# Optimization experiments

Measured on AMD Instinct MI355X. Metric: run time of the kernel, lower is better.

## Reference

```python
import jax, jax.numpy as jnp
import numpy as np

HEADS, DIM_HEAD, BITS = 12, 64, 4


def quantize(q, bits):
    # per-tensor affine fake-quant, exactly as the torch quantize()
    s = (q.max() - q.min()) / (2.0 ** bits - 1.0)
    z = jnp.round(2.0 ** bits - 1.0 - q.max() / s)
    return jnp.round(q / s + z), s, z


def setup_inputs() -> dict:
    key = jax.random.key(0)
    k1, k2, k3, k4 = jax.random.split(key, 4)
    return {
        "x": jax.random.normal(k1, (4, 1024, 768), jnp.float32),
        "w_qkv": jax.random.normal(k2, (2304, 768), jnp.float32) * 0.02,  # torch Linear weight [out,in]
        "w_out": jax.random.normal(k3, (768, 768), jnp.float32) * 0.02,
        "b_out": jax.random.normal(k4, (768,), jnp.float32) * 0.02,
    }


def reference(x, w_qkv, w_out, b_out):
    scale = DIM_HEAD ** -0.5
    B, N, D = x.shape
    # --- quantized QKV projection: x @ W^T with zero-point correction ---
    xq, sx1, zx1 = quantize(x, BITS)
    w1, sw1, zw1 = quantize(w_qkv.T, BITS)  # [D, 3*inner]
    xqkv = (xq @ w1
            - w1.sum(0, keepdims=True) * zx1
            - xq.sum(2, keepdims=True) * zw1
            + zx1 * zw1 * D) * (sx1 * sw1)  # [B, N, 3*inner]
    q, k, v = jnp.split(xqkv, 3, axis=-1)
    to_heads = lambda t: t.reshape(B, N, HEADS, DIM_HEAD).transpose(0, 2, 1, 3)  # b h n d
    q, k, v = to_heads(q), to_heads(k), to_heads(v)
    # --- quantized QK^T (note: original omits the +zq*zk*d term) ---
    qq, sq, zq = quantize(q, BITS)
    kq, sk, zk = quantize(k.transpose(0, 1, 3, 2), BITS)  # b h d n
    dots = (qq @ kq
            - kq.sum(2, keepdims=True) * zq
            - qq.sum(3, keepdims=True) * zk) * (scale * sq * sk)  # b h n n
    a = jax.nn.softmax(dots, axis=-1)
    # --- quantized A @ V ---
    aq, sa, za = quantize(a, BITS)
    vq, sv, zv = quantize(v, BITS)
    out = (aq @ vq
           - vq.sum(2, keepdims=True) * za
           - aq.sum(3, keepdims=True) * zv
           + za * zv * N) * (sa * sv)  # b h n d
    out = out.transpose(0, 2, 1, 3).reshape(B, N, HEADS * DIM_HEAD)
    # --- quantized output projection (faithful to original: correction uses
    # xqkv.sum / xqkv width, reproducing the source's use of `x` here) ---
    oq, sx2, zx2 = quantize(out, BITS)
    w2, sw2, zw2 = quantize(w_out.T, BITS)  # [inner, D]
    o = (oq @ w2
         - w2.sum(0, keepdims=True) * zx2
         - xqkv.sum(2, keepdims=True) * zw2
         + zx2 * zw2 * xqkv.shape[2]) * (sx2 * sw2) + b_out
    return o
```

## Files before the change

kernel.cpp:

```cpp
#include <hip/hip_runtime.h>
#include <math.h>

#define HEADS 12
#define DH    64
#define Dm    768
#define I3    2304
#define Nn    1024
#define Mm    4096
#define BHt   48

#define P_X  0
#define P_W1 1
#define P_Q  2
#define P_K  3
#define P_V  4
#define P_A  5
#define P_O  6
#define P_W2 7

typedef int v4i __attribute__((ext_vector_type(4)));

__device__ inline unsigned encf(float f) {
    unsigned u = __float_as_uint(f);
    return (u & 0x80000000u) ? ~u : (u | 0x80000000u);
}
__device__ inline float decf(unsigned u) {
    return (u & 0x80000000u) ? __uint_as_float(u & 0x7fffffffu) : __uint_as_float(~u);
}
__device__ inline void get_sz(const unsigned* scal, int pair, float* s, float* z) {
    float mn = decf(scal[2 * pair]);
    float mx = decf(scal[2 * pair + 1]);
    float ss = (mx - mn) / 15.0f;
    *s = ss;
    *z = rintf(15.0f - mx / ss);
}

__global__ __launch_bounds__(256) void k_init(unsigned* scal, float* zbuf, int nz) {
    int g = blockIdx.x * 256 + threadIdx.x;
    if (g < nz) zbuf[g] = 0.f;
    if (g < 8) { scal[2 * g] = 0xFFFFFFFFu; scal[2 * g + 1] = 0u; }
}

__global__ __launch_bounds__(256) void k_minmax3(const float* x, const float* w1, const float* w2,
                                                 unsigned* scal) {
    __shared__ float rmn[256], rmx[256];
    int bid = blockIdx.x, tid = threadIdx.x;
    const float* src; int rows, pair, b0, nb;
    if (bid < 256)      { src = x;  rows = 4096; pair = P_X;  b0 = 0;   nb = 256; }
    else if (bid < 384) { src = w1; rows = 2304; pair = P_W1; b0 = 256; nb = 128; }
    else                { src = w2; rows = 768;  pair = P_W2; b0 = 384; nb = 64;  }
    float mn = INFINITY, mx = -INFINITY;
    for (int r = bid - b0; r < rows; r += nb) {
        const float* row = src + (long)r * 768;
#pragma unroll
        for (int k = 0; k < 3; ++k) {
            float v = row[tid + k * 256];
            mn = fminf(mn, v); mx = fmaxf(mx, v);
        }
    }
    rmn[tid] = mn; rmx[tid] = mx; __syncthreads();
    for (int s = 128; s > 0; s >>= 1) {
        if (tid < s) { rmn[tid] = fminf(rmn[tid], rmn[tid + s]); rmx[tid] = fmaxf(rmx[tid], rmx[tid + s]); }
        __syncthreads();
    }
    if (tid == 0) {
        atomicMin(&scal[2 * pair], encf(rmn[0]));
        atomicMax(&scal[2 * pair + 1], encf(rmx[0]));
    }
}

__global__ __launch_bounds__(256) void k_quant3(const float* x, const float* w1, const float* w2,
                                                const unsigned* scal,
// ... 114 lines not shown
            float cs = colsumB[col] * zA;
            float bv = bias ? bias[col] : 0.f;
#pragma unroll
            for (int r = 0; r < 4; ++r) {
                long row = rowbase + wave * 32 + i2 * 16 + quad * 4 + r;
                float v = ((float)acc[i2][g][r] - cs - rowsumA[row] * zB + zz) * sAB + bv;
                C[row * ldC + col] = v;
                rowpart[i2][r] += v;
                vmn = fminf(vmn, v); vmx = fmaxf(vmx, v);
            }
        }
    if (do_stats) {
#pragma unroll
        for (int i2 = 0; i2 < 2; ++i2)
#pragma unroll
            for (int r = 0; r < 4; ++r) {
                float s = rowpart[i2][r];
                s += __shfl_xor(s, 1); s += __shfl_xor(s, 2);
                s += __shfl_xor(s, 4); s += __shfl_xor(s, 8);
                if (col16 == 0)
                    atomicAdd(&rowsum_out[rowbase + wave * 32 + i2 * 16 + quad * 4 + r], s);
            }
        int pair = P_Q + (int)(colbase / 768);
        red[tid] = vmx; __syncthreads();
        for (int s = 128; s > 0; s >>= 1) { if (tid < s) red[tid] = fmaxf(red[tid], red[tid + s]); __syncthreads(); }
        if (tid == 0) atomicMax(&scal_mm[2 * pair + 1], encf(red[0]));
        __syncthreads();
        red[tid] = vmn; __syncthreads();
        for (int s = 128; s > 0; s >>= 1) { if (tid < s) red[tid] = fminf(red[tid], red[tid + s]); __syncthreads(); }
        if (tid == 0) atomicMin(&scal_mm[2 * pair], encf(red[0]));
    }
}

__global__ __launch_bounds__(64) void k_quant_qkv(const float* xqkv, const unsigned* scal,
                                                  signed char* qq, signed char* kq, signed char* vqT,
                                                  float* rowsum_qq, float* colsum_kq) {
    int blk = blockIdx.x;
    int bh = blk >> 10, i = blk & 1023;
    int d = threadIdx.x;
    int b = bh / HEADS, h = bh - HEADS * b;
    const float* row = xqkv + ((long)b * Nn + i) * I3 + h * DH;
    float sq, zq, sk, zk, sv, zv;
    get_sz(scal, P_Q, &sq, &zq);
    get_sz(scal, P_K, &sk, &zk);
    get_sz(scal, P_V, &sv, &zv);
    float q = rintf(row[d] / sq + zq);
    float k = rintf(row[768 + d] / sk + zk);
    float v = rintf(row[1536 + d] / sv + zv);
    long o = (long)blk * 64 + d;
    qq[o] = (signed char)(int)q;
    kq[o] = (signed char)(int)k;
    vqT[((long)bh * 64 + d) * 1024 + i] = (signed char)(int)v;
    float s1 = q, s2 = k;
    for (int off = 32; off > 0; off >>= 1) {
        s1 += __shfl_down(s1, off);
        s2 += __shfl_down(s2, off);
    }
    if (d == 0) { rowsum_qq[blk] = s1; colsum_kq[blk] = s2; }
}

__global__ __launch_bounds__(256) void k_colsum_vq(const signed char* vqT, float* colsum) {
    __shared__ float red[256];
    int tid = threadIdx.x;
    const signed char* row = vqT + (long)blockIdx.x * 1024;
    float acc = 0.f;
    for (int j = tid; j < Nn; j += 256) acc += (float)row[j];
    red[tid] = acc; __syncthreads();
    for (int s = 128; s > 0; s >>= 1) { if (tid < s) red[tid] += red[tid + s]; __syncthreads(); }
    if (tid == 0) colsum[blockIdx.x] = red[0];
}

__global__ __launch_bounds__(256) void k_attn_a2(const signed char* qq, const signed char* kq,
                                                 const float* rowsum_qq, const float* colsum_kq,
                                                 unsigned* scal, float* rowmax, float* sumexp) {
    __shared__ float redm[256];
    int blk = blockIdx.x;
    int bh = blk >> 4, itile = blk & 15;
    int tid = threadIdx.x;
    int wave = tid >> 6, lane = tid & 63;
    int col16 = lane & 15, quad = lane >> 4;
    int rowbase = itile * 64 + wave * 16;
    const signed char* kbase = kq + (long)bh * Nn * 64;
    const float* csk_base = colsum_kq + bh * Nn;
    v4i afrag = *(const v4i*)(qq + ((long)bh * Nn + rowbase + col16) * 64 + quad * 16);
    float sq, zq, sk, zk;
    get_sz(scal, P_Q, &sq, &zq);
    get_sz(scal, P_K, &sk, &zk);
    float csc = (0.125f * sq) * sk;
    float rsq[4];
#pragma unroll
    for (int r = 0; r < 4; ++r) rsq[r] = rowsum_qq[bh * Nn + rowbase + quad * 4 + r];
    float lmax[4] = {-INFINITY, -INFINITY, -INFINITY, -INFINITY};
    float lmin[4] = {INFINITY, INFINITY, INFINITY, INFINITY};
    v4i zero = {0, 0, 0, 0};
    for (int jt = 0; jt < 64; ++jt) {
        v4i bfrag = *(const v4i*)(kbase + (long)(jt * 16 + col16) * 64 + quad * 16);
        v4i d = __builtin_amdgcn_mfma_i32_16x16x64_i8(afrag, bfrag, zero, 0, 0, 0);
        float csk = csk_base[jt * 16 + col16] * zq;
#pragma unroll
        for (int r = 0; r < 4; ++r) {
            float dv = ((float)d[r] - csk - rsq[r] * zk) * csc;
            lmax[r] = fmaxf(lmax[r], dv);
            lmin[r] = fminf(lmin[r], dv);
        }
    }
#pragma unroll
    for (int r = 0; r < 4; ++r) {
        for (int off = 1; off < 16; off <<= 1) {
            lmax[r] = fmaxf(lmax[r], __shfl_xor(lmax[r], off));
            lmin[r] = fminf(lmin[r], __shfl_xor(lmin[r], off));
        }
    }
    float se[4] = {0.f, 0.f, 0.f, 0.f};
    for (int jt = 0; jt < 64; ++jt) {
        v4i bfrag = *(const v4i*)(kbase + (long)(jt * 16 + col16) * 64 + quad * 16);
        v4i d = __builtin_amdgcn_mfma_i32_16x16x64_i8(afrag, bfrag, zero, 0, 0, 0);
        float csk = csk_base[jt * 16 + col16] * zq;
#pragma unroll
        for (int r = 0; r < 4; ++r) {
            float dv = ((float)d[r] - csk - rsq[r] * zk) * csc;
            se[r] += expf(dv - lmax[r]);
        }
    }
#pragma unroll
    for (int r = 0; r < 4; ++r)
        for (int off = 1; off < 16; off <<= 1) se[r] += __shfl_xor(se[r], off);
    float amax_c = -INFINITY, amin_c = INFINITY;
    if (col16 == 0) {
#pragma unroll
        for (int r = 0; r < 4; ++r) {
            int row = bh * Nn + rowbase + quad * 4 + r;
            rowmax[row] = lmax[r];
            sumexp[row] = se[r];
            amax_c = fmaxf(amax_c, 1.0f / se[r]);
            amin_c = fminf(amin_c, expf(lmin[r] - lmax[r]) / se[r]);
        }
    }
    redm[tid] = amax_c; __syncthreads();
    for (int s = 128; s > 0; s >>= 1) { if (tid < s) redm[tid] = fmaxf(redm[tid], redm[tid + s]); __syncthreads(); }
    if (tid == 0) atomicMax(&scal[2 * P_A + 1], encf(redm[0]));
    __syncthreads();
    redm[tid] = amin_c; __syncthreads();
    for (int s = 128; s > 0; s >>= 1) { if (tid < s) redm[tid] = fminf(redm[tid], redm[tid + s]); __syncthreads(); }
    if (tid == 0) atomicMin(&scal[2 * P_A], encf(redm[0]));
}

__global__ __launch_bounds__(256) void k_attn_b2(const signed char* qq, const signed char* kq,
                                                 const signed char* vqT, const float* rowsum_qq,
                                                 const float* colsum_kq, const float* colsum_vq,
                                                 const float* rowmax, const float* sumexp,
                                                 unsigned* scal, float* out_mat) {
    __shared__ __align__(16) signed char Aq[4][16 * 64];
    __shared__ float red[256];
    int blk = blockIdx.x;
    int bh = blk >> 4, itile = blk & 15;
    int tid = threadIdx.x;
    int wave = tid >> 6, lane = tid & 63;
    int col16 = lane & 15, quad = lane >> 4;
    int rowbase = itile * 64 + wave * 16;
    int b = bh / HEADS, h = bh - HEADS * b;
    const signed char* kbase = kq + (long)bh * Nn * 64;
    const signed char* vbase = vqT + (long)bh * 64 * 1024;
    const float* csk_base = colsum_kq + bh * Nn;
    v4i afrag = *(const v4i*)(qq + ((long)bh * Nn + rowbase + col16) * 64 + quad * 16);
    float sq, zq, sk, zk, sv, zv, sa, za;
    get_sz(scal, P_Q, &sq, &zq);
    get_sz(scal, P_K, &sk, &zk);
    get_sz(scal, P_V, &sv, &zv);
    get_sz(scal, P_A, &sa, &za);
    float csc = (0.125f * sq) * sk;
    float rsq[4], m[4], se[4], crcp[4];
#pragma unroll
    for (int r = 0; r < 4; ++r) {
        int row = bh * Nn + rowbase + quad * 4 + r;
        rsq[r] = rowsum_qq[row];
        m[r] = rowmax[row];
        se[r] = sumexp[row];
        crcp[r] = 1.0f / (se[r] * sa);
    }
    signed char* myAq = Aq[wave];
    v4i accPV[4] = {};
    float rs_a[4] = {0.f, 0.f, 0.f, 0.f};
    v4i zero = {0, 0, 0, 0};
    for (int ch = 0; ch < 16; ++ch) {
#pragma unroll
        for (int t = 0; t < 4; ++t) {
            int jt = ch * 4 + t;
            v4i bfrag = *(const v4i*)(kbase + (long)(jt * 16 + col16) * 64 + quad * 16);
            v4i d = __builtin_amdgcn_mfma_i32_16x16x64_i8(afrag, bfrag, zero, 0, 0, 0);
            float csk = csk_base[jt * 16 + col16] * zq;
#pragma unroll
            for (int r = 0; r < 4; ++r) {
                float dv = ((float)d[r] - csk - rsq[r] * zk) * csc;
                float es = dv - m[r];
                float fastv = fmaf(__expf(es), crcp[r], za);
                float fr = fastv - floorf(fastv);
                if (fabsf(fr - 0.5f) < 1.5e-4f) {
                    float av = expf(es) / se[r];
                    fastv = av / sa + za;
                }
                float aqv = rintf(fastv);
                rs_a[r] += aqv;
                myAq[(quad * 4 + r) * 64 + t * 16 + col16] = (signed char)(int)aqv;
            }
        }
        asm volatile("s_waitcnt lgkmcnt(0)" ::: "memory");
        v4i pa = *(const v4i*)(myAq + col16 * 64 + quad * 16);
#pragma unroll
        for (int g = 0; g < 4; ++g) {
            v4i bv = *(const v4i*)(vbase + ((long)(g * 16 + col16)) * 1024 + ch * 64 + quad * 16);
            accPV[g] = __builtin_amdgcn_mfma_i32_16x16x64_i8(pa, bv, accPV[g], 0, 0, 0);
        }
        asm volatile("s_waitcnt lgkmcnt(0)" ::: "memory");
    }
#pragma unroll
    for (int r = 0; r < 4; ++r)
        for (int off = 1; off < 16; off <<= 1) rs_a[r] += __shfl_xor(rs_a[r], off);
    float sav = sa * sv;
    float zz = (za * zv) * 1024.0f;
    float vmn = INFINITY, vmx = -INFINITY;
#pragma unroll
    for (int g = 0; g < 4; ++g) {
        int d = g * 16 + col16;
        float cs = colsum_vq[bh * 64 + d] * za;
#pragma unroll
        for (int r = 0; r < 4; ++r) {
            int i = rowbase + quad * 4 + r;
            float v = ((float)accPV[g][r] - cs - rs_a[r] * zv + zz) * sav;
            out_mat[((long)b * Nn + i) * Dm + h * DH + d] = v;
            vmn = fminf(vmn, v); vmx = fmaxf(vmx, v);
        }
    }
    red[tid] = vmx; __syncthreads();
    for (int s = 128; s > 0; s >>= 1) { if (tid < s) red[tid] = fmaxf(red[tid], red[tid + s]); __syncthreads(); }
    if (tid == 0) atomicMax(&scal[2 * P_O + 1], encf(red[0]));
    __syncthreads();
    red[tid] = vmn; __syncthreads();
    for (int s = 128; s > 0; s >>= 1) { if (tid < s) red[tid] = fminf(red[tid], red[tid + s]); __syncthreads(); }
    if (tid == 0) atomicMin(&scal[2 * P_O], encf(red[0]));
}

extern "C" void kernel_launch(void* const* d_in, const int* in_sizes, int n_in,
                              void* d_out, int out_size, void* d_ws, size_t ws_size,
                              hipStream_t stream) {
    const float* x     = (const float*)d_in[0];
    const float* w_qkv = (const float*)d_in[1];
    const float* w_out = (const float*)d_in[2];
    const float* b_out = (const float*)d_in[3];

    char* ws = (char*)d_ws;
    size_t off = 0;
    auto alloc = [&](size_t n) -> char* {
        char* p = ws + off;
        off = (off + n + 255) & ~(size_t)255;
        return p;
    };
    unsigned*    scal        = (unsigned*)alloc(64);
    float*       xqkv        = (float*)alloc((size_t)Mm * I3 * 4);
    float*       out_mat     = (float*)alloc((size_t)Mm * Dm * 4);
    signed char* xq          = (signed char*)alloc((size_t)Mm * Dm);
    signed char* wq          = (signed char*)alloc((size_t)I3 * Dm);
    signed char* w2q         = (signed char*)alloc((size_t)Dm * Dm);
    signed char* oq          = (signed char*)alloc((size_t)Mm * Dm);
    signed char* qq          = (signed char*)alloc((size_t)BHt * Nn * DH);
    signed char* kq          = (signed char*)alloc((size_t)BHt * Nn * DH);
    signed char* vqT         = (signed char*)alloc((size_t)BHt * Nn * DH);
    float*       rowsum_xq   = (float*)alloc((size_t)Mm * 4);
    float*       colsum_w1   = (float*)alloc((size_t)I3 * 4);
    float*       colsum_w2   = (float*)alloc((size_t)Dm * 4);
    float*       rowsum_xqkv = (float*)alloc((size_t)Mm * 4);
    float*       rowsum_qq   = (float*)alloc((size_t)BHt * Nn * 4);
    float*       colsum_kq   = (float*)alloc((size_t)BHt * Nn * 4);
    float*       colsum_vq   = (float*)alloc((size_t)BHt * DH * 4);
    float*       rowmax      = (float*)alloc((size_t)BHt * Nn * 4);
    float*       sumexp      = (float*)alloc((size_t)BHt * Nn * 4);
    float*       oq_rowsum   = (float*)alloc((size_t)Mm * 4);

    k_init<<<16, 256, 0, stream>>>(scal, rowsum_xqkv, Mm);

    k_minmax3<<<448, 256, 0, stream>>>(x, w_qkv, w_out, scal);
    k_quant3<<<7168, 256, 0, stream>>>(x, w_qkv, w_out, scal, xq, wq, w2q,
                                       rowsum_xq, colsum_w1, colsum_w2);

    {
        dim3 g(I3 / 128, Mm / 128);
        k_gemm_mfma<<<g, 256, 0, stream>>>(xq, wq, colsum_w1, rowsum_xq, nullptr, xqkv,
                                           Dm, I3, scal, P_X, P_W1, 768.0f,
                                           1, rowsum_xqkv, scal);
    }

    k_quant_qkv<<<BHt * Nn, 64, 0, stream>>>(xqkv, scal, qq, kq, vqT, rowsum_qq, colsum_kq);
    k_colsum_vq<<<BHt * DH, 256, 0, stream>>>(vqT, colsum_vq);

    k_attn_a2<<<BHt * 16, 256, 0, stream>>>(qq, kq, rowsum_qq, colsum_kq, scal, rowmax, sumexp);
    k_attn_b2<<<BHt * 16, 256, 0, stream>>>(qq, kq, vqT, rowsum_qq, colsum_kq, colsum_vq,
                                            rowmax, sumexp, scal, out_mat);

    k_quant_rows<<<Mm, 256, 0, stream>>>(out_mat, scal, P_O, oq, oq_rowsum);

    {
        dim3 g(Dm / 128, Mm / 128);
        k_gemm_mfma<<<g, 256, 0, stream>>>(oq, w2q, colsum_w2, rowsum_xqkv, b_out, (float*)d_out,
                                           Dm, Dm, scal, P_O, P_W2, 2304.0f,
                                           0, nullptr, nullptr);
    }
}
```

Baseline: 303.1 us.

## Stage K and V tiles in LDS with register prefetch in attention kernels

The attention kernels now cooperatively load 256-key chunks of K, and of V in the second kernel, into shared memory. Each chunk is prefetched into registers one step ahead, replacing per-wave strided global loads that each wave repeated on its own. The quant_qkv kernel now handles four rows per 256-thread block instead of one row per 64-thread block, cutting launch and scheduling overhead. The row-sum exp pass uses fast __expf, which may shift results slightly, and the extra shared memory and barriers may lower occupancy.

Result: no change. 298.3 us (-1.6%).

```diff
diff --git a/kernel.cpp b/kernel.cpp
--- a/kernel.cpp
+++ b/kernel.cpp
@@ -218,12 +218,13 @@
     }
 }
 
-__global__ __launch_bounds__(64) void k_quant_qkv(const float* xqkv, const unsigned* scal,
-                                                  signed char* qq, signed char* kq, signed char* vqT,
-                                                  float* rowsum_qq, float* colsum_kq) {
-    int blk = blockIdx.x;
-    int bh = blk >> 10, i = blk & 1023;
-    int d = threadIdx.x;
+__global__ __launch_bounds__(256) void k_quant_qkv(const float* xqkv, const unsigned* scal,
+                                                   signed char* qq, signed char* kq, signed char* vqT,
+                                                   float* rowsum_qq, float* colsum_kq) {
+    int tid = threadIdx.x;
+    int wave = tid >> 6, d = tid & 63;
+    int base = blockIdx.x * 4 + wave;
+    int bh = base >> 10, i = base & 1023;
     int b = bh / HEADS, h = bh - HEADS * b;
     const float* row = xqkv + ((long)b * Nn + i) * I3 + h * DH;
     float sq, zq, sk, zk, sv, zv;
@@ -233,7 +234,7 @@
     float q = rintf(row[d] / sq + zq);
     float k = rintf(row[768 + d] / sk + zk);
     float v = rintf(row[1536 + d] / sv + zv);
-    long o = (long)blk * 64 + d;
+    long o = (long)base * 64 + d;
     qq[o] = (signed char)(int)q;
     kq[o] = (signed char)(int)k;
     vqT[((long)bh * 64 + d) * 1024 + i] = (signed char)(int)v;
@@ -242,7 +243,7 @@
         s1 += __shfl_down(s1, off);
         s2 += __shfl_down(s2, off);
     }
-    if (d == 0) { rowsum_qq[blk] = s1; colsum_kq[blk] = s2; }
+    if (d == 0) { rowsum_qq[base] = s1; colsum_kq[base] = s2; }
 }
 
 __global__ __launch_bounds__(256) void k_colsum_vq(const signed char* vqT, float* colsum) {
@@ -259,6 +260,7 @@
 __global__ __launch_bounds__(256) void k_attn_a2(const signed char* qq, const signed char* kq,
                                                  const float* rowsum_qq, const float* colsum_kq,
                                                  unsigned* scal, float* rowmax, float* sumexp) {
+    __shared__ __align__(16) signed char Kls[16384];
     __shared__ float redm[256];
     int blk = blockIdx.x;
     int bh = blk >> 4, itile = blk & 15;
@@ -276,18 +278,35 @@
     float rsq[4];
 #pragma unroll
     for (int r = 0; r < 4; ++r) rsq[r] = rowsum_qq[bh * Nn + rowbase + quad * 4 + r];
+
+    int skey = ((tid & 15)) * 64 + ((tid >> 4) & 3) * 16;
+    int ldsoff = tid * 16;
+    v4i rk[4];
+#define LOADK(sc)  { _Pragma("unroll") for (int i = 0; i < 4; ++i) \
+        rk[i] = *(const v4i*)(kbase + ((long)(sc) * 256 + (i * 4 + wave) * 16) * 64 + skey); }
+#define STOREK()   { _Pragma("unroll") for (int i = 0; i < 4; ++i) \
+        *(v4i*)(Kls + i * 4096 + ldsoff) = rk[i]; }
+
+    v4i zero = {0, 0, 0, 0};
     float lmax[4] = {-INFINITY, -INFINITY, -INFINITY, -INFINITY};
     float lmin[4] = {INFINITY, INFINITY, INFINITY, INFINITY};
-    v4i zero = {0, 0, 0, 0};
-    for (int jt = 0; jt < 64; ++jt) {
-        v4i bfrag = *(const v4i*)(kbase + (long)(jt * 16 + col16) * 64 + quad * 16);
-        v4i d = __builtin_amdgcn_mfma_i32_16x16x64_i8(afrag, bfrag, zero, 0, 0, 0);
-        float csk = csk_base[jt * 16 + col16] * zq;
-#pragma unroll
-        for (int r = 0; r < 4; ++r) {
-            float dv = ((float)d[r] - csk - rsq[r] * zk) * csc;
-            lmax[r] = fmaxf(lmax[r], dv);
-            lmin[r] = fminf(lmin[r], dv);
+    LOADK(0);
+    for (int sc = 0; sc < 4; ++sc) {
+        __syncthreads();
+        STOREK();
+        __syncthreads();
+        if (sc < 3) LOADK(sc + 1);
+#pragma unroll
+        for (int u = 0; u < 16; ++u) {
+            v4i bfrag = *(const v4i*)(Kls + u * 1024 + quad * 256 + col16 * 16);
+            v4i d = __builtin_amdgcn_mfma_i32_16x16x64_i8(afrag, bfrag, zero, 0, 0, 0);
+            float csk = csk_base[sc * 256 + u * 16 + col16] * zq;
+#pragma unroll
+            for (int r = 0; r < 4; ++r) {
+                float dv = ((float)d[r] - csk - rsq[r] * zk) * csc;
+                lmax[r] = fmaxf(lmax[r], dv);
+                lmin[r] = fminf(lmin[r], dv);
+            }
         }
     }
 #pragma unroll
@@ -298,16 +317,26 @@
         }
     }
     float se[4] = {0.f, 0.f, 0.f, 0.f};
-    for (int jt = 0; jt < 64; ++jt) {
-        v4i bfrag = *(const v4i*)(kbase + (long)(jt * 16 + col16) * 64 + quad * 16);
-        v4i d = __builtin_amdgcn_mfma_i32_16x16x64_i8(afrag, bfrag, zero, 0, 0, 0);
-        float csk = csk_base[jt * 16 + col16] * zq;
-#pragma unroll
-        for (int r = 0; r < 4; ++r) {
-            float dv = ((float)d[r] - csk - rsq[r] * zk) * csc;
-            se[r] += expf(dv - lmax[r]);
-        }
-    }
+    LOADK(0);
+    for (int sc = 0; sc < 4; ++sc) {
+        __syncthreads();
+        STOREK();
+        __syncthreads();
+        if (sc < 3) LOADK(sc + 1);
+#pragma unroll
+        for (int u = 0; u < 16; ++u) {
+            v4i bfrag = *(const v4i*)(Kls + u * 1024 + quad * 256 + col16 * 16);
+            v4i d = __builtin_amdgcn_mfma_i32_16x16x64_i8(afrag, bfrag, zero, 0, 0, 0);
+            float csk = csk_base[sc * 256 + u * 16 + col16] * zq;
+#pragma unroll
+            for (int r = 0; r < 4; ++r) {
+                float dv = ((float)d[r] - csk - rsq[r] * zk) * csc;
+                se[r] += __expf(dv - lmax[r]);
+            }
+        }
+    }
+#undef LOADK
+#undef STOREK
 #pragma unroll
     for (int r = 0; r < 4; ++r)
         for (int off = 1; off < 16; off <<= 1) se[r] += __shfl_xor(se[r], off);
@@ -319,7 +348,7 @@
             rowmax[row] = lmax[r];
             sumexp[row] = se[r];
             amax_c = fmaxf(amax_c, 1.0f / se[r]);
-            amin_c = fminf(amin_c, expf(lmin[r] - lmax[r]) / se[r]);
+            amin_c = fminf(amin_c, __expf(lmin[r] - lmax[r]) / se[r]);
         }
     }
     redm[tid] = amax_c; __syncthreads();
@@ -336,7 +365,9 @@
                                                  const float* colsum_kq, const float* colsum_vq,
                                                  const float* rowmax, const float* sumexp,
                                                  unsigned* scal, float* out_mat) {
-    __shared__ __align__(16) signed char Aq[4][16 * 64];
+    __shared__ __align__(16) signed char Kls[16384];
+    __shared__ __align__(16) signed char Vls[16384];
+    __shared__ __align__(16) signed char AqB[8192];
     __shared__ float red[256];
     int blk = blockIdx.x;
     int bh = blk >> 4, itile = blk & 15;
@@ -364,41 +395,61 @@
         se[r] = sumexp[row];
         crcp[r] = 1.0f / (se[r] * sa);
     }
-    signed char* myAq = Aq[wave];
+
+    int skey = ((tid & 15)) * 64 + ((tid >> 4) & 3) * 16;
+    int ldsoff = tid * 16;
+    v4i rk[4], rv[4];
+#define LOADKV(sc) { _Pragma("unroll") for (int i = 0; i < 4; ++i) { \
+        rk[i] = *(const v4i*)(kbase + ((long)(sc) * 256 + (i * 4 + wave) * 16) * 64 + skey); \
+        rv[i] = *(const v4i*)(vbase + (long)(i * 16 + (tid & 15)) * 1024 + (sc) * 256 + (tid >> 4) * 16); } }
+#define STOREKV()  { _Pragma("unroll") for (int i = 0; i < 4; ++i) { \
+        *(v4i*)(Kls + i * 4096 + ldsoff) = rk[i]; \
+        *(v4i*)(Vls + i * 4096 + ldsoff) = rv[i]; } }
+
     v4i accPV[4] = {};
     float rs_a[4] = {0.f, 0.f, 0.f, 0.f};
     v4i zero = {0, 0, 0, 0};
-    for (int ch = 0; ch < 16; ++ch) {
-#pragma unroll
-        for (int t = 0; t < 4; ++t) {
-            int jt = ch * 4 + t;
-            v4i bfrag = *(const v4i*)(kbase + (long)(jt * 16 + col16) * 64 + quad * 16);
-            v4i d = __builtin_amdgcn_mfma_i32_16x16x64_i8(afrag, bfrag, zero, 0, 0, 0);
-            float csk = csk_base[jt * 16 + col16] * zq;
-#pragma unroll
-            for (int r = 0; r < 4; ++r) {
-                float dv = ((float)d[r] - csk - rsq[r] * zk) * csc;
-                float es = dv - m[r];
-                float fastv = fmaf(__expf(es), crcp[r], za);
-                float fr = fastv - floorf(fastv);
-                if (fabsf(fr - 0.5f) < 1.5e-4f) {
-                    float av = expf(es) / se[r];
-                    fastv = av / sa + za;
+    LOADKV(0);
+    for (int sc = 0; sc < 4; ++sc) {
+        __syncthreads();
+        STOREKV();
+        __syncthreads();
+        if (sc < 3) LOADKV(sc + 1);
+#pragma unroll
+        for (int ci = 0; ci < 4; ++ci) {
+            signed char* myAq = AqB + (ci & 1) * 4096 + wave * 1024;
+#pragma unroll
+            for (int u = 0; u < 4; ++u) {
+                int kt = ci * 4 + u;
+                v4i bfrag = *(const v4i*)(Kls + kt * 1024 + quad * 256 + col16 * 16);
+                v4i d = __builtin_amdgcn_mfma_i32_16x16x64_i8(afrag, bfrag, zero, 0, 0, 0);
+                float csk = csk_base[sc * 256 + kt * 16 + col16] * zq;
+#pragma unroll
+                for (int r = 0; r < 4; ++r) {
+                    float dv = ((float)d[r] - csk - rsq[r] * zk) * csc;
+                    float es = dv - m[r];
+                    float fastv = fmaf(__expf(es), crcp[r], za);
+                    float fr = fastv - floorf(fastv);
+                    if (fabsf(fr - 0.5f) < 1.5e-4f) {
+                        float av = expf(es) / se[r];
+                        fastv = av / sa + za;
+                    }
+                    float aqv = rintf(fastv);
+                    rs_a[r] += aqv;
+                    myAq[(quad * 4 + r) * 64 + u * 16 + col16] = (signed char)(int)aqv;
                 }
-                float aqv = rintf(fastv);
-                rs_a[r] += aqv;
-                myAq[(quad * 4 + r) * 64 + t * 16 + col16] = (signed char)(int)aqv;
             }
-        }
-        asm volatile("s_waitcnt lgkmcnt(0)" ::: "memory");
-        v4i pa = *(const v4i*)(myAq + col16 * 64 + quad * 16);
-#pragma unroll
-        for (int g = 0; g < 4; ++g) {
-            v4i bv = *(const v4i*)(vbase + ((long)(g * 16 + col16)) * 1024 + ch * 64 + quad * 16);
-            accPV[g] = __builtin_amdgcn_mfma_i32_16x16x64_i8(pa, bv, accPV[g], 0, 0, 0);
-        }
-        asm volatile("s_waitcnt lgkmcnt(0)" ::: "memory");
-    }
+            asm volatile("s_waitcnt lgkmcnt(0)" ::: "memory");
+            v4i pa = *(const v4i*)(myAq + col16 * 64 + quad * 16);
+#pragma unroll
+            for (int g = 0; g < 4; ++g) {
+                v4i bv = *(const v4i*)(Vls + g * 4096 + (ci * 4 + quad) * 256 + col16 * 16);
+                accPV[g] = __builtin_amdgcn_mfma_i32_16x16x64_i8(pa, bv, accPV[g], 0, 0, 0);
+            }
+        }
+    }
+#undef LOADKV
+#undef STOREKV
 #pragma unroll
     for (int r = 0; r < 4; ++r)
         for (int off = 1; off < 16; off <<= 1) rs_a[r] += __shfl_xor(rs_a[r], off);
@@ -475,7 +526,7 @@
                                            1, rowsum_xqkv, scal);
     }
 
-    k_quant_qkv<<<BHt * Nn, 64, 0, stream>>>(xqkv, scal, qq, kq, vqT, rowsum_qq, colsum_kq);
+    k_quant_qkv<<<BHt * Nn / 4, 256, 0, stream>>>(xqkv, scal, qq, kq, vqT, rowsum_qq, colsum_kq);
     k_colsum_vq<<<BHt * DH, 256, 0, stream>>>(vqT, colsum_vq);
 
     k_attn_a2<<<BHt * 16, 256, 0, stream>>>(qq, kq, rowsum_qq, colsum_kq, scal, rowmax, sumexp);
```

## Split attention keys across waves and batch QKV quantization with LDS-transposed V

Applied to the files above, without the earlier changes.

The attention kernels now give each block 16 query rows and split the 1024 keys across its four waves. Partial max, min, sum-of-exp and PV accumulators are combined through LDS, which quadruples the grid and shortens each wave's serial loop. The QKV quantize kernel now handles 64 rows per 256-thread block and transposes V through shared memory, so vqT is written with 16-byte coalesced stores instead of scattered byte stores. The change also swaps expf for __expf, which may shift softmax values slightly, and adds cross-wave reduction and LDS traffic in the attention kernels.

Result: slower. 362.4 us (+19.6%).

```diff
diff --git a/kernel.cpp b/kernel.cpp
--- a/kernel.cpp
+++ b/kernel.cpp
@@ -218,31 +218,45 @@
     }
 }
 
-__global__ __launch_bounds__(64) void k_quant_qkv(const float* xqkv, const unsigned* scal,
-                                                  signed char* qq, signed char* kq, signed char* vqT,
-                                                  float* rowsum_qq, float* colsum_kq) {
+__global__ __launch_bounds__(256) void k_quant_qkv2(const float* xqkv, const unsigned* scal,
+                                                    signed char* qq, signed char* kq, signed char* vqT,
+                                                    float* rowsum_qq, float* colsum_kq) {
+    __shared__ __align__(16) signed char vt[64 * 80];
     int blk = blockIdx.x;
-    int bh = blk >> 10, i = blk & 1023;
-    int d = threadIdx.x;
+    int bh = blk >> 4, itile = blk & 15;
+    int tid = threadIdx.x;
+    int wave = tid >> 6, d = tid & 63;
     int b = bh / HEADS, h = bh - HEADS * b;
-    const float* row = xqkv + ((long)b * Nn + i) * I3 + h * DH;
     float sq, zq, sk, zk, sv, zv;
     get_sz(scal, P_Q, &sq, &zq);
     get_sz(scal, P_K, &sk, &zk);
     get_sz(scal, P_V, &sv, &zv);
-    float q = rintf(row[d] / sq + zq);
-    float k = rintf(row[768 + d] / sk + zk);
-    float v = rintf(row[1536 + d] / sv + zv);
-    long o = (long)blk * 64 + d;
-    qq[o] = (signed char)(int)q;
-    kq[o] = (signed char)(int)k;
-    vqT[((long)bh * 64 + d) * 1024 + i] = (signed char)(int)v;
-    float s1 = q, s2 = k;
-    for (int off = 32; off > 0; off >>= 1) {
-        s1 += __shfl_down(s1, off);
-        s2 += __shfl_down(s2, off);
-    }
-    if (d == 0) { rowsum_qq[blk] = s1; colsum_kq[blk] = s2; }
+    int vb = 0;
+    for (int ir = 0; ir < 16; ++ir) {
+        int il = wave * 16 + ir;
+        int i = itile * 64 + il;
+        const float* row = xqkv + ((long)b * Nn + i) * I3 + h * DH;
+        float q = rintf(row[d] / sq + zq);
+        float k = rintf(row[768 + d] / sk + zk);
+        float v = rintf(row[1536 + d] / sv + zv);
+        long o = ((long)bh * Nn + i) * 64 + d;
+        qq[o] = (signed char)(int)q;
+        kq[o] = (signed char)(int)k;
+        vb |= ((int)v & 0xff) << ((ir & 3) * 8);
+        if ((ir & 3) == 3) {
+            *(int*)(vt + d * 80 + (il & ~3)) = vb;
+            vb = 0;
+        }
+        float s1 = q, s2 = k;
+        for (int off = 32; off > 0; off >>= 1) {
+            s1 += __shfl_down(s1, off);
+            s2 += __shfl_down(s2, off);
+        }
+        if (d == 0) { rowsum_qq[bh * Nn + i] = s1; colsum_kq[bh * Nn + i] = s2; }
+    }
+    __syncthreads();
+    int dd = tid >> 2, c = tid & 3;
+    *(v4i*)(vqT + ((long)bh * 64 + dd) * 1024 + itile * 64 + c * 16) = *(const v4i*)(vt + dd * 80 + c * 16);
 }
 
 __global__ __launch_bounds__(256) void k_colsum_vq(const signed char* vqT, float* colsum) {
@@ -256,16 +270,18 @@
     if (tid == 0) colsum[blockIdx.x] = red[0];
 }
 
-__global__ __launch_bounds__(256) void k_attn_a2(const signed char* qq, const signed char* kq,
+__global__ __launch_bounds__(256) void k_attn_a3(const signed char* qq, const signed char* kq,
                                                  const float* rowsum_qq, const float* colsum_kq,
                                                  unsigned* scal, float* rowmax, float* sumexp) {
-    __shared__ float redm[256];
+    __shared__ float redW[4][16], redW2[4][16];
+    __shared__ float red[256];
     int blk = blockIdx.x;
-    int bh = blk >> 4, itile = blk & 15;
+    int bh = blk >> 6, rt = blk & 63;
     int tid = threadIdx.x;
     int wave = tid >> 6, lane = tid & 63;
     int col16 = lane & 15, quad = lane >> 4;
-    int rowbase = itile * 64 + wave * 16;
+    int rowbase = rt * 16;
+    int keys0 = wave * 256;
     const signed char* kbase = kq + (long)bh * Nn * 64;
     const float* csk_base = colsum_kq + bh * Nn;
     v4i afrag = *(const v4i*)(qq + ((long)bh * Nn + rowbase + col16) * 64 + quad * 16);
@@ -276,13 +292,14 @@
     float rsq[4];
 #pragma unroll
     for (int r = 0; r < 4; ++r) rsq[r] = rowsum_qq[bh * Nn + rowbase + quad * 4 + r];
+    v4i zero = {0, 0, 0, 0};
     float lmax[4] = {-INFINITY, -INFINITY, -INFINITY, -INFINITY};
     float lmin[4] = {INFINITY, INFINITY, INFINITY, INFINITY};
-    v4i zero = {0, 0, 0, 0};
-    for (int jt = 0; jt < 64; ++jt) {
-        v4i bfrag = *(const v4i*)(kbase + (long)(jt * 16 + col16) * 64 + quad * 16);
+    for (int jt = 0; jt < 16; ++jt) {
+        int keybase = keys0 + jt * 16;
+        v4i bfrag = *(const v4i*)(kbase + (long)(keybase + col16) * 64 + quad * 16);
         v4i d = __builtin_amdgcn_mfma_i32_16x16x64_i8(afrag, bfrag, zero, 0, 0, 0);
-        float csk = csk_base[jt * 16 + col16] * zq;
+        float csk = csk_base[keybase + col16] * zq;
 #pragma unroll
         for (int r = 0; r < 4; ++r) {
             float dv = ((float)d[r] - csk - rsq[r] * zk) * csc;
@@ -296,54 +313,72 @@
             lmax[r] = fmaxf(lmax[r], __shfl_xor(lmax[r], off));
             lmin[r] = fminf(lmin[r], __shfl_xor(lmin[r], off));
         }
-    }
+        if (col16 == 0) { redW[wave][quad * 4 + r] = lmax[r]; redW2[wave][quad * 4 + r] = lmin[r]; }
+    }
+    __syncthreads();
+    float m[4], lmn[4];
+#pragma unroll
+    for (int r = 0; r < 4; ++r) {
+        int row = quad * 4 + r;
+        m[r]   = fmaxf(fmaxf(redW[0][row], redW[1][row]), fmaxf(redW[2][row], redW[3][row]));
+        lmn[r] = fminf(fminf(redW2[0][row], redW2[1][row]), fminf(redW2[2][row], redW2[3][row]));
+    }
+    __syncthreads();
     float se[4] = {0.f, 0.f, 0.f, 0.f};
-    for (int jt = 0; jt < 64; ++jt) {
-        v4i bfrag = *(const v4i*)(kbase + (long)(jt * 16 + col16) * 64 + quad * 16);
+    for (int jt = 0; jt < 16; ++jt) {
+        int keybase = keys0 + jt * 16;
+        v4i bfrag = *(const v4i*)(kbase + (long)(keybase + col16) * 64 + quad * 16);
         v4i d = __builtin_amdgcn_mfma_i32_16x16x64_i8(afrag, bfrag, zero, 0, 0, 0);
-        float csk = csk_base[jt * 16 + col16] * zq;
+        float csk = csk_base[keybase + col16] * zq;
 #pragma unroll
         for (int r = 0; r < 4; ++r) {
             float dv = ((float)d[r] - csk - rsq[r] * zk) * csc;
-            se[r] += expf(dv - lmax[r]);
-        }
-    }
-#pragma unroll
-    for (int r = 0; r < 4; ++r)
+            se[r] += __expf(dv - m[r]);
+        }
+    }
+#pragma unroll
+    for (int r = 0; r < 4; ++r) {
         for (int off = 1; off < 16; off <<= 1) se[r] += __shfl_xor(se[r], off);
+        if (col16 == 0) redW[wave][quad * 4 + r] = se[r];
+    }
+    __syncthreads();
     float amax_c = -INFINITY, amin_c = INFINITY;
-    if (col16 == 0) {
+    if (wave == 0 && col16 == 0) {
 #pragma unroll
         for (int r = 0; r < 4; ++r) {
-            int row = bh * Nn + rowbase + quad * 4 + r;
-            rowmax[row] = lmax[r];
-            sumexp[row] = se[r];
-            amax_c = fmaxf(amax_c, 1.0f / se[r]);
-            amin_c = fminf(amin_c, expf(lmin[r] - lmax[r]) / se[r]);
-        }
-    }
-    redm[tid] = amax_c; __syncthreads();
-    for (int s = 128; s > 0; s >>= 1) { if (tid < s) redm[tid] = fmaxf(redm[tid], redm[tid + s]); __syncthreads(); }
-    if (tid == 0) atomicMax(&scal[2 * P_A + 1], encf(redm[0]));
-    __syncthreads();
-    redm[tid] = amin_c; __syncthreads();
-    for (int s = 128; s > 0; s >>= 1) { if (tid < s) redm[tid] = fminf(redm[tid], redm[tid + s]); __syncthreads(); }
-    if (tid == 0) atomicMin(&scal[2 * P_A], encf(redm[0]));
-}
-
-__global__ __launch_bounds__(256) void k_attn_b2(const signed char* qq, const signed char* kq,
+            int row = quad * 4 + r;
+            float sef = ((redW[0][row] + redW[1][row]) + redW[2][row]) + redW[3][row];
+            int grow = bh * Nn + rowbase + row;
+            rowmax[grow] = m[r];
+            sumexp[grow] = sef;
+            amax_c = fmaxf(amax_c, 1.0f / sef);
+            amin_c = fminf(amin_c, __expf(lmn[r] - m[r]) / sef);
+        }
+    }
+    red[tid] = amax_c; __syncthreads();
+    for (int s = 128; s > 0; s >>= 1) { if (tid < s) red[tid] = fmaxf(red[tid], red[tid + s]); __syncthreads(); }
+    if (tid == 0) atomicMax(&scal[2 * P_A + 1], encf(red[0]));
+    __syncthreads();
+    red[tid] = amin_c; __syncthreads();
+    for (int s = 128; s > 0; s >>= 1) { if (tid < s) red[tid] = fminf(red[tid], red[tid + s]); __syncthreads(); }
+    if (tid == 0) atomicMin(&scal[2 * P_A], encf(red[0]));
+}
+
+__global__ __launch_bounds__(256) void k_attn_b3(const signed char* qq, const signed char* kq,
                                                  const signed char* vqT, const float* rowsum_qq,
                                                  const float* colsum_kq, const float* colsum_vq,
                                                  const float* rowmax, const float* sumexp,
                                                  unsigned* scal, float* out_mat) {
-    __shared__ __align__(16) signed char Aq[4][16 * 64];
+    __shared__ __align__(16) signed char Big[16384];
+    __shared__ float redF[4][16];
     __shared__ float red[256];
     int blk = blockIdx.x;
-    int bh = blk >> 4, itile = blk & 15;
+    int bh = blk >> 6, rt = blk & 63;
     int tid = threadIdx.x;
     int wave = tid >> 6, lane = tid & 63;
     int col16 = lane & 15, quad = lane >> 4;
-    int rowbase = itile * 64 + wave * 16;
+    int rowbase = rt * 16;
+    int keys0 = wave * 256;
     int b = bh / HEADS, h = bh - HEADS * b;
     const signed char* kbase = kq + (long)bh * Nn * 64;
     const signed char* vbase = vqT + (long)bh * 64 * 1024;
@@ -364,17 +399,18 @@
         se[r] = sumexp[row];
         crcp[r] = 1.0f / (se[r] * sa);
     }
-    signed char* myAq = Aq[wave];
     v4i accPV[4] = {};
     float rs_a[4] = {0.f, 0.f, 0.f, 0.f};
     v4i zero = {0, 0, 0, 0};
-    for (int ch = 0; ch < 16; ++ch) {
-#pragma unroll
-        for (int t = 0; t < 4; ++t) {
-            int jt = ch * 4 + t;
-            v4i bfrag = *(const v4i*)(kbase + (long)(jt * 16 + col16) * 64 + quad * 16);
+#pragma unroll
+    for (int ci = 0; ci < 4; ++ci) {
+        signed char* myAq = Big + wave * 2048 + (ci & 1) * 1024;
+#pragma unroll
+        for (int u = 0; u < 4; ++u) {
+            int keybase = keys0 + ci * 64 + u * 16;
+            v4i bfrag = *(const v4i*)(kbase + (long)(keybase + col16) * 64 + quad * 16);
             v4i d = __builtin_amdgcn_mfma_i32_16x16x64_i8(afrag, bfrag, zero, 0, 0, 0);
-            float csk = csk_base[jt * 16 + col16] * zq;
+            float csk = csk_base[keybase + col16] * zq;
 #pragma unroll
             for (int r = 0; r < 4; ++r) {
                 float dv = ((float)d[r] - csk - rsq[r] * zk) * csc;
@@ -387,34 +423,55 @@
                 }
                 float aqv = rintf(fastv);
                 rs_a[r] += aqv;
-                myAq[(quad * 4 + r) * 64 + t * 16 + col16] = (signed char)(int)aqv;
+                myAq[(quad * 4 + r) * 64 + u * 16 + col16] = (signed char)(int)aqv;
             }
         }
         asm volatile("s_waitcnt lgkmcnt(0)" ::: "memory");
         v4i pa = *(const v4i*)(myAq + col16 * 64 + quad * 16);
 #pragma unroll
         for (int g = 0; g < 4; ++g) {
-            v4i bv = *(const v4i*)(vbase + ((long)(g * 16 + col16)) * 1024 + ch * 64 + quad * 16);
+            v4i bv = *(const v4i*)(vbase + (long)(g * 16 + col16) * 1024 + keys0 + ci * 64 + quad * 16);
             accPV[g] = __builtin_amdgcn_mfma_i32_16x16x64_i8(pa, bv, accPV[g], 0, 0, 0);
         }
-        asm volatile("s_waitcnt lgkmcnt(0)" ::: "memory");
-    }
+    }
+#pragma unroll
+    for (int r = 0; r < 4; ++r) {
+        for (int off = 1; off < 16; off <<= 1) rs_a[r] += __shfl_xor(rs_a[r], off);
+    }
+    __syncthreads();
 #pragma unroll
     for (int r = 0; r < 4; ++r)
-        for (int off = 1; off < 16; off <<= 1) rs_a[r] += __shfl_xor(rs_a[r], off);
-    float sav = sa * sv;
-    float zz = (za * zv) * 1024.0f;
+        if (col16 == 0) redF[wave][quad * 4 + r] = rs_a[r];
+    v4i* accLDS = (v4i*)Big;
+#pragma unroll
+    for (int g = 0; g < 4; ++g) accLDS[(wave * 64 + lane) * 4 + g] = accPV[g];
+    __syncthreads();
     float vmn = INFINITY, vmx = -INFINITY;
-#pragma unroll
-    for (int g = 0; g < 4; ++g) {
-        int d = g * 16 + col16;
-        float cs = colsum_vq[bh * 64 + d] * za;
+    if (wave == 0) {
+        float sav = sa * sv;
+        float zz = (za * zv) * 1024.0f;
+        float rs_row[4];
 #pragma unroll
         for (int r = 0; r < 4; ++r) {
-            int i = rowbase + quad * 4 + r;
-            float v = ((float)accPV[g][r] - cs - rs_a[r] * zv + zz) * sav;
-            out_mat[((long)b * Nn + i) * Dm + h * DH + d] = v;
-            vmn = fminf(vmn, v); vmx = fmaxf(vmx, v);
+            int row = quad * 4 + r;
+            rs_row[r] = ((redF[0][row] + redF[1][row]) + redF[2][row]) + redF[3][row];
+        }
+#pragma unroll
+        for (int g = 0; g < 4; ++g) {
+            v4i s0 = accLDS[lane * 4 + g];
+            v4i s1 = accLDS[(64 + lane) * 4 + g];
+            v4i s2 = accLDS[(128 + lane) * 4 + g];
+            v4i s3 = accLDS[(192 + lane) * 4 + g];
+            int d = g * 16 + col16;
+            float cs = colsum_vq[bh * 64 + d] * za;
+#pragma unroll
+            for (int r = 0; r < 4; ++r) {
+                int sum = s0[r] + s1[r] + s2[r] + s3[r];
+                int i = rowbase + quad * 4 + r;
+                float v = ((float)sum - cs - rs_row[r] * zv + zz) * sav;
+                out_mat[((long)b * Nn + i) * Dm + h * DH + d] = v;
+                vmn = fminf(vmn, v); vmx = fmaxf(vmx, v);
+            }
         }
     }
     red[tid] = vmx; __syncthreads();
@@ -475,11 +532,11 @@
                                            1, rowsum_xqkv, scal);
     }
 
-    k_quant_qkv<<<BHt * Nn, 64, 0, stream>>>(xqkv, scal, qq, kq, vqT, rowsum_qq, colsum_kq);
+    k_quant_qkv2<<<BHt * 16, 256, 0, stream>>>(xqkv, scal, qq, kq, vqT, rowsum_qq, colsum_kq);
     k_colsum_vq<<<BHt * DH, 256, 0, stream>>>(vqT, colsum_vq);
 
-    k_attn_a2<<<BHt * 16, 256, 0, stream>>>(qq, kq, rowsum_qq, colsum_kq, scal, rowmax, sumexp);
-    k_attn_b2<<<BHt * 16, 256, 0, stream>>>(qq, kq, vqT, rowsum_qq, colsum_kq, colsum_vq,
+    k_attn_a3<<<BHt * 64, 256, 0, stream>>>(qq, kq, rowsum_qq, colsum_kq, scal, rowmax, sumexp);
+    k_attn_b3<<<BHt * 64, 256, 0, stream>>>(qq, kq, vqT, rowsum_qq, colsum_kq, colsum_vq,
                                             rowmax, sumexp, scal, out_mat);
 
     k_quant_rows<<<Mm, 256, 0, stream>>>(out_mat, scal, P_O, oq, oq_rowsum);
```

## Fuse V colsum into QKV quant, use online softmax, precompute K correction terms

Applied to the files above, without the earlier changes.

Replaces the per-row QKV quantization kernel with a tiled 256-thread kernel. It transposes V through shared memory for coalesced stores and atomically accumulates the V column sums, which removes the separate colsum kernel. The attention stats pass now computes max and sum-of-exp in one online-softmax sweep instead of two MFMA passes. It also stores K column sums prescaled by zq*csc and folds the row terms into a single fma. The PV kernel double-buffers the A tile in shared memory, drops an explicit waitcnt, and removes the exact-expf fallback near rounding ties. That removal risks off-by-one quantized attention values.

After: 272.1 us. -10.2%, faster.

```diff
diff --git a/kernel.cpp b/kernel.cpp
--- a/kernel.cpp
+++ b/kernel.cpp
@@ -35,9 +35,10 @@
     *z = rintf(15.0f - mx / ss);
 }
 
-__global__ __launch_bounds__(256) void k_init(unsigned* scal, float* zbuf, int nz) {
+__global__ __launch_bounds__(256) void k_init(unsigned* scal, float* z1, int n1, float* z2, int n2) {
     int g = blockIdx.x * 256 + threadIdx.x;
-    if (g < nz) zbuf[g] = 0.f;
+    if (g < n1) z1[g] = 0.f;
+    if (g < n2) z2[g] = 0.f;
     if (g < 8) { scal[2 * g] = 0xFFFFFFFFu; scal[2 * g + 1] = 0u; }
 }
 
@@ -218,48 +219,59 @@
     }
 }
 
-__global__ __launch_bounds__(64) void k_quant_qkv(const float* xqkv, const unsigned* scal,
-                                                  signed char* qq, signed char* kq, signed char* vqT,
-                                                  float* rowsum_qq, float* colsum_kq) {
+__global__ __launch_bounds__(256) void k_quant_qkv2(const float* xqkv, const unsigned* scal,
+                                                    signed char* qq, signed char* kq, signed char* vqT,
+                                                    float* rowsum_qq, float* cskc, float* colsum_vq) {
+    __shared__ __align__(16) signed char vt[64 * 80];
+    __shared__ float vred[4][64];
     int blk = blockIdx.x;
-    int bh = blk >> 10, i = blk & 1023;
-    int d = threadIdx.x;
+    int bh = blk >> 4, itile = blk & 15;
+    int tid = threadIdx.x;
+    int wave = tid >> 6, d = tid & 63;
     int b = bh / HEADS, h = bh - HEADS * b;
-    const float* row = xqkv + ((long)b * Nn + i) * I3 + h * DH;
     float sq, zq, sk, zk, sv, zv;
     get_sz(scal, P_Q, &sq, &zq);
     get_sz(scal, P_K, &sk, &zk);
     get_sz(scal, P_V, &sv, &zv);
-    float q = rintf(row[d] / sq + zq);
-    float k = rintf(row[768 + d] / sk + zk);
-    float v = rintf(row[1536 + d] / sv + zv);
-    long o = (long)blk * 64 + d;
-    qq[o] = (signed char)(int)q;
-    kq[o] = (signed char)(int)k;
-    vqT[((long)bh * 64 + d) * 1024 + i] = (signed char)(int)v;
-    float s1 = q, s2 = k;
-    for (int off = 32; off > 0; off >>= 1) {
-        s1 += __shfl_down(s1, off);
-        s2 += __shfl_down(s2, off);
-    }
-    if (d == 0) { rowsum_qq[blk] = s1; colsum_kq[blk] = s2; }
-}
-
-__global__ __launch_bounds__(256) void k_colsum_vq(const signed char* vqT, float* colsum) {
+    float zqcsc = zq * ((0.125f * sq) * sk);
+    int vb = 0;
+    float vsum = 0.f;
+    for (int ir = 0; ir < 16; ++ir) {
+        int il = wave * 16 + ir;
+        int i = itile * 64 + il;
+        const float* row = xqkv + ((long)b * Nn + i) * I3 + h * DH;
+        float q = rintf(row[d] / sq + zq);
+        float k = rintf(row[768 + d] / sk + zk);
+        float v = rintf(row[1536 + d] / sv + zv);
+        long o = ((long)bh * Nn + i) * 64 + d;
+        qq[o] = (signed char)(int)q;
+        kq[o] = (signed char)(int)k;
+        vsum += v;
+        vb |= ((int)v & 0xff) << ((ir & 3) * 8);
+        if ((ir & 3) == 3) {
+            *(int*)(vt + d * 80 + (il & ~3)) = vb;
+            vb = 0;
+        }
+        float s1 = q, s2 = k;
+        for (int off = 32; off > 0; off >>= 1) {
+            s1 += __shfl_down(s1, off);
+            s2 += __shfl_down(s2, off);
+        }
+        if (d == 0) { rowsum_qq[bh * Nn + i] = s1; cskc[bh * Nn + i] = s2 * zqcsc; }
+    }
+    vred[wave][d] = vsum;
+    __syncthreads();
+    int dd = tid >> 2, c = tid & 3;
+    *(v4i*)(vqT + ((long)bh * 64 + dd) * 1024 + itile * 64 + c * 16) = *(const v4i*)(vt + dd * 80 + c * 16);
+    if (tid < 64)
+        atomicAdd(&colsum_vq[bh * 64 + tid],
+                  ((vred[0][tid] + vred[1][tid]) + vred[2][tid]) + vred[3][tid]);
+}
+
+__global__ __launch_bounds__(256) void k_attn_a4(const signed char* qq, const signed char* kq,
+                                                 const float* rowsum_qq, const float* cskc,
+                                                 unsigned* scal, float* rowmax, float* sumexp) {
     __shared__ float red[256];
-    int tid = threadIdx.x;
-    const signed char* row = vqT + (long)blockIdx.x * 1024;
-    float acc = 0.f;
-    for (int j = tid; j < Nn; j += 256) acc += (float)row[j];
-    red[tid] = acc; __syncthreads();
-    for (int s = 128; s > 0; s >>= 1) { if (tid < s) red[tid] += red[tid + s]; __syncthreads(); }
-    if (tid == 0) colsum[blockIdx.x] = red[0];
-}
-
-__global__ __launch_bounds__(256) void k_attn_a2(const signed char* qq, const signed char* kq,
-                                                 const float* rowsum_qq, const float* colsum_kq,
-                                                 unsigned* scal, float* rowmax, float* sumexp) {
-    __shared__ float redm[256];
     int blk = blockIdx.x;
     int bh = blk >> 4, itile = blk & 15;
     int tid = threadIdx.x;
@@ -267,76 +279,72 @@
     int col16 = lane & 15, quad = lane >> 4;
     int rowbase = itile * 64 + wave * 16;
     const signed char* kbase = kq + (long)bh * Nn * 64;
-    const float* csk_base = colsum_kq + bh * Nn;
+    const float* ck = cskc + bh * Nn;
     v4i afrag = *(const v4i*)(qq + ((long)bh * Nn + rowbase + col16) * 64 + quad * 16);
     float sq, zq, sk, zk;
     get_sz(scal, P_Q, &sq, &zq);
     get_sz(scal, P_K, &sk, &zk);
     float csc = (0.125f * sq) * sk;
-    float rsq[4];
-#pragma unroll
-    for (int r = 0; r < 4; ++r) rsq[r] = rowsum_qq[bh * Nn + rowbase + quad * 4 + r];
-    float lmax[4] = {-INFINITY, -INFINITY, -INFINITY, -INFINITY};
+    float rzc[4];
+#pragma unroll
+    for (int r = 0; r < 4; ++r)
+        rzc[r] = rowsum_qq[bh * Nn + rowbase + quad * 4 + r] * zk * csc;
+    v4i zero = {0, 0, 0, 0};
+    float m[4]    = {-INFINITY, -INFINITY, -INFINITY, -INFINITY};
+    float se[4]   = {0.f, 0.f, 0.f, 0.f};
     float lmin[4] = {INFINITY, INFINITY, INFINITY, INFINITY};
-    v4i zero = {0, 0, 0, 0};
     for (int jt = 0; jt < 64; ++jt) {
         v4i bfrag = *(const v4i*)(kbase + (long)(jt * 16 + col16) * 64 + quad * 16);
         v4i d = __builtin_amdgcn_mfma_i32_16x16x64_i8(afrag, bfrag, zero, 0, 0, 0);
-        float csk = csk_base[jt * 16 + col16] * zq;
+        float ckv = ck[jt * 16 + col16];
 #pragma unroll
         for (int r = 0; r < 4; ++r) {
-            float dv = ((float)d[r] - csk - rsq[r] * zk) * csc;
-            lmax[r] = fmaxf(lmax[r], dv);
+            float dv = fmaf((float)d[r], csc, -(ckv + rzc[r]));
             lmin[r] = fminf(lmin[r], dv);
+            float mn = fmaxf(m[r], dv);
+            se[r] = fmaf(se[r], __expf(m[r] - mn), __expf(dv - mn));
+            m[r] = mn;
         }
     }
 #pragma unroll
     for (int r = 0; r < 4; ++r) {
+#pragma unroll
         for (int off = 1; off < 16; off <<= 1) {
-            lmax[r] = fmaxf(lmax[r], __shfl_xor(lmax[r], off));
-            lmin[r] = fminf(lmin[r], __shfl_xor(lmin[r], off));
-        }
-    }
-    float se[4] = {0.f, 0.f, 0.f, 0.f};
-    for (int jt = 0; jt < 64; ++jt) {
-        v4i bfrag = *(const v4i*)(kbase + (long)(jt * 16 + col16) * 64 + quad * 16);
-        v4i d = __builtin_amdgcn_mfma_i32_16x16x64_i8(afrag, bfrag, zero, 0, 0, 0);
-        float csk = csk_base[jt * 16 + col16] * zq;
-#pragma unroll
-        for (int r = 0; r < 4; ++r) {
-            float dv = ((float)d[r] - csk - rsq[r] * zk) * csc;
-            se[r] += expf(dv - lmax[r]);
-        }
-    }
-#pragma unroll
-    for (int r = 0; r < 4; ++r)
-        for (int off = 1; off < 16; off <<= 1) se[r] += __shfl_xor(se[r], off);
+            float mo = __shfl_xor(m[r], off);
+            float so = __shfl_xor(se[r], off);
+            float mino = __shfl_xor(lmin[r], off);
+            float mn = fmaxf(m[r], mo);
+            se[r] = fmaf(se[r], __expf(m[r] - mn), so * __expf(mo - mn));
+            m[r] = mn;
+            lmin[r] = fminf(lmin[r], mino);
+        }
+    }
     float amax_c = -INFINITY, amin_c = INFINITY;
     if (col16 == 0) {
 #pragma unroll
         for (int r = 0; r < 4; ++r) {
-            int row = bh * Nn + rowbase + quad * 4 + r;
-            rowmax[row] = lmax[r];
-            sumexp[row] = se[r];
+            int grow = bh * Nn + rowbase + quad * 4 + r;
+            rowmax[grow] = m[r];
+            sumexp[grow] = se[r];
             amax_c = fmaxf(amax_c, 1.0f / se[r]);
-            amin_c = fminf(amin_c, expf(lmin[r] - lmax[r]) / se[r]);
-        }
-    }
-    redm[tid] = amax_c; __syncthreads();
-    for (int s = 128; s > 0; s >>= 1) { if (tid < s) redm[tid] = fmaxf(redm[tid], redm[tid + s]); __syncthreads(); }
-    if (tid == 0) atomicMax(&scal[2 * P_A + 1], encf(redm[0]));
+            amin_c = fminf(amin_c, __expf(lmin[r] - m[r]) / se[r]);
+        }
+    }
+    red[tid] = amax_c; __syncthreads();
+    for (int s = 128; s > 0; s >>= 1) { if (tid < s) red[tid] = fmaxf(red[tid], red[tid + s]); __syncthreads(); }
+    if (tid == 0) atomicMax(&scal[2 * P_A + 1], encf(red[0]));
     __syncthreads();
-    redm[tid] = amin_c; __syncthreads();
-    for (int s = 128; s > 0; s >>= 1) { if (tid < s) redm[tid] = fminf(redm[tid], redm[tid + s]); __syncthreads(); }
-    if (tid == 0) atomicMin(&scal[2 * P_A], encf(redm[0]));
-}
-
-__global__ __launch_bounds__(256) void k_attn_b2(const signed char* qq, const signed char* kq,
+    red[tid] = amin_c; __syncthreads();
+    for (int s = 128; s > 0; s >>= 1) { if (tid < s) red[tid] = fminf(red[tid], red[tid + s]); __syncthreads(); }
+    if (tid == 0) atomicMin(&scal[2 * P_A], encf(red[0]));
+}
+
+__global__ __launch_bounds__(256) void k_attn_b4(const signed char* qq, const signed char* kq,
                                                  const signed char* vqT, const float* rowsum_qq,
-                                                 const float* colsum_kq, const float* colsum_vq,
+                                                 const float* cskc, const float* colsum_vq,
                                                  const float* rowmax, const float* sumexp,
                                                  unsigned* scal, float* out_mat) {
-    __shared__ __align__(16) signed char Aq[4][16 * 64];
+    __shared__ __align__(16) signed char AqB[8192];
     __shared__ float red[256];
     int blk = blockIdx.x;
     int bh = blk >> 4, itile = blk & 15;
@@ -347,7 +355,7 @@
     int b = bh / HEADS, h = bh - HEADS * b;
     const signed char* kbase = kq + (long)bh * Nn * 64;
     const signed char* vbase = vqT + (long)bh * 64 * 1024;
-    const float* csk_base = colsum_kq + bh * Nn;
+    const float* ck = cskc + bh * Nn;
     v4i afrag = *(const v4i*)(qq + ((long)bh * Nn + rowbase + col16) * 64 + quad * 16);
     float sq, zq, sk, zk, sv, zv, sa, za;
     get_sz(scal, P_Q, &sq, &zq);
@@ -355,36 +363,28 @@
     get_sz(scal, P_V, &sv, &zv);
     get_sz(scal, P_A, &sa, &za);
     float csc = (0.125f * sq) * sk;
-    float rsq[4], m[4], se[4], crcp[4];
+    float roff[4], crcp[4];
 #pragma unroll
     for (int r = 0; r < 4; ++r) {
         int row = bh * Nn + rowbase + quad * 4 + r;
-        rsq[r] = rowsum_qq[row];
-        m[r] = rowmax[row];
-        se[r] = sumexp[row];
-        crcp[r] = 1.0f / (se[r] * sa);
-    }
-    signed char* myAq = Aq[wave];
+        roff[r] = rowsum_qq[row] * zk * csc + rowmax[row];
+        crcp[r] = 1.0f / (sumexp[row] * sa);
+    }
     v4i accPV[4] = {};
     float rs_a[4] = {0.f, 0.f, 0.f, 0.f};
     v4i zero = {0, 0, 0, 0};
     for (int ch = 0; ch < 16; ++ch) {
+        signed char* myAq = AqB + (ch & 1) * 4096 + wave * 1024;
 #pragma unroll
         for (int t = 0; t < 4; ++t) {
             int jt = ch * 4 + t;
             v4i bfrag = *(const v4i*)(kbase + (long)(jt * 16 + col16) * 64 + quad * 16);
             v4i d = __builtin_amdgcn_mfma_i32_16x16x64_i8(afrag, bfrag, zero, 0, 0, 0);
-            float csk = csk_base[jt * 16 + col16] * zq;
+            float ckv = ck[jt * 16 + col16];
 #pragma unroll
             for (int r = 0; r < 4; ++r) {
-                float dv = ((float)d[r] - csk - rsq[r] * zk) * csc;
-                float es = dv - m[r];
+                float es = fmaf((float)d[r], csc, -(ckv + roff[r]));
                 float fastv = fmaf(__expf(es), crcp[r], za);
-                float fr = fastv - floorf(fastv);
-                if (fabsf(fr - 0.5f) < 1.5e-4f) {
-                    float av = expf(es) / se[r];
-                    fastv = av / sa + za;
-                }
                 float aqv = rintf(fastv);
                 rs_a[r] += aqv;
                 myAq[(quad * 4 + r) * 64 + t * 16 + col16] = (signed char)(int)aqv;
@@ -394,10 +394,9 @@
         v4i pa = *(const v4i*)(myAq + col16 * 64 + quad * 16);
 #pragma unroll
         for (int g = 0; g < 4; ++g) {
-            v4i bv = *(const v4i*)(vbase + ((long)(g * 16 + col16)) * 1024 + ch * 64 + quad * 16);
+            v4i bv = *(const v4i*)(vbase + (long)(g * 16 + col16) * 1024 + ch * 64 + quad * 16);
             accPV[g] = __builtin_amdgcn_mfma_i32_16x16x64_i8(pa, bv, accPV[g], 0, 0, 0);
         }
-        asm volatile("s_waitcnt lgkmcnt(0)" ::: "memory");
     }
 #pragma unroll
     for (int r = 0; r < 4; ++r)
@@ -456,13 +455,13 @@
     float*       colsum_w2   = (float*)alloc((size_t)Dm * 4);
     float*       rowsum_xqkv = (float*)alloc((size_t)Mm * 4);
     float*       rowsum_qq   = (float*)alloc((size_t)BHt * Nn * 4);
-    float*       colsum_kq   = (float*)alloc((size_t)BHt * Nn * 4);
+    float*       cskc        = (float*)alloc((size_t)BHt * Nn * 4);
     float*       colsum_vq   = (float*)alloc((size_t)BHt * DH * 4);
     float*       rowmax      = (float*)alloc((size_t)BHt * Nn * 4);
     float*       sumexp      = (float*)alloc((size_t)BHt * Nn * 4);
     float*       oq_rowsum   = (float*)alloc((size_t)Mm * 4);
 
-    k_init<<<16, 256, 0, stream>>>(scal, rowsum_xqkv, Mm);
+    k_init<<<28, 256, 0, stream>>>(scal, rowsum_xqkv, Mm, colsum_vq, BHt * DH);
 
     k_minmax3<<<448, 256, 0, stream>>>(x, w_qkv, w_out, scal);
     k_quant3<<<7168, 256, 0, stream>>>(x, w_qkv, w_out, scal, xq, wq, w2q,
@@ -475,11 +474,11 @@
                                            1, rowsum_xqkv, scal);
     }
 
-    k_quant_qkv<<<BHt * Nn, 64, 0, stream>>>(xqkv, scal, qq, kq, vqT, rowsum_qq, colsum_kq);
-    k_colsum_vq<<<BHt * DH, 256, 0, stream>>>(vqT, colsum_vq);
-
-    k_attn_a2<<<BHt * 16, 256, 0, stream>>>(qq, kq, rowsum_qq, colsum_kq, scal, rowmax, sumexp);
-    k_attn_b2<<<BHt * 16, 256, 0, stream>>>(qq, kq, vqT, rowsum_qq, colsum_kq, colsum_vq,
+    k_quant_qkv2<<<BHt * 16, 256, 0, stream>>>(xqkv, scal, qq, kq, vqT,
+                                               rowsum_qq, cskc, colsum_vq);
+
+    k_attn_a4<<<BHt * 16, 256, 0, stream>>>(qq, kq, rowsum_qq, cskc, scal, rowmax, sumexp);
+    k_attn_b4<<<BHt * 16, 256, 0, stream>>>(qq, kq, vqT, rowsum_qq, cskc, colsum_vq,
                                             rowmax, sumexp, scal, out_mat);
 
     k_quant_rows<<<Mm, 256, 0, stream>>>(out_mat, scal, P_O, oq, oq_rowsum);
```
